# Optimization experiments

Hardware: AMD Instinct MI355X
Metric: run time of the kernel (lower is better)

## Reference

```python
import jax, jax.numpy as jnp
import numpy as np

B, T, DIN, P, HID, L = 256, 512, 25, 128, 256, 5
Q = 0.15
EPS = 1e-5


def setup_inputs() -> dict:
    key = jax.random.key(0)
    ks = jax.random.split(key, 12)
    s = 0.05
    return {
        "x": jax.random.normal(ks[0], (B, T, DIN), jnp.float32),
        "lengths": jax.random.randint(ks[1], (B,), 1, T + 1),
        "ln_g": jnp.ones((DIN,), jnp.float32),
        "ln_b": jnp.zeros((DIN,), jnp.float32),
        "w1": jax.random.normal(ks[2], (DIN, P), jnp.float32) * s,
        "b1": jnp.zeros((P,), jnp.float32),
        "w2": jax.random.normal(ks[3], (P, P), jnp.float32) * s,
        "b2": jnp.zeros((P,), jnp.float32),
        "Wih0": jax.random.normal(ks[4], (2, 3 * HID, P), jnp.float32) * s,
        "Whh0": jax.random.normal(ks[5], (2, 3 * HID, HID), jnp.float32) * s,
        "bih0": jnp.zeros((2, 3 * HID), jnp.float32),
        "bhh0": jnp.zeros((2, 3 * HID), jnp.float32),
        "Wih": jax.random.normal(ks[6], (L - 1, 2, 3 * HID, 2 * HID), jnp.float32) * s,
        "Whh": jax.random.normal(ks[7], (L - 1, 2, 3 * HID, HID), jnp.float32) * s,
        "bih": jnp.zeros((L - 1, 2, 3 * HID), jnp.float32),
        "bhh": jnp.zeros((L - 1, 2, 3 * HID), jnp.float32),
        "Wc": jax.random.normal(ks[8], (2 * HID,), jnp.float32) * s,
        "bc": jnp.zeros((), jnp.float32),
    }


def _gru_dir(xs, mask, Wih, Whh, bih, bhh):
    """Masked unidirectional GRU (PyTorch gate convention). xs:[B,T,Din], mask:[B,T] -> [B,T,HID]."""
    xw = jnp.einsum('btd,gd->btg', xs, Wih) + bih  # [B,T,3H] precomputed input gates

    def step(h, inp):
        xw_t, m_t = inp  # [B,3H], [B]
        gh = h @ Whh.T + bhh
        r = jax.nn.sigmoid(xw_t[:, :HID] + gh[:, :HID])
        z = jax.nn.sigmoid(xw_t[:, HID:2 * HID] + gh[:, HID:2 * HID])
        n = jnp.tanh(xw_t[:, 2 * HID:] + r * gh[:, 2 * HID:])
        h_new = (1.0 - z) * n + z * h
        h = jnp.where(m_t[:, None], h_new, h)        # hold state past sequence end (packing)
        return h, jnp.where(m_t[:, None], h, 0.0)    # padded outputs are zero (pad_packed)

    h0 = jnp.zeros((xs.shape[0], HID), xs.dtype)
    _, ys = jax.lax.scan(step, h0, (xw.transpose(1, 0, 2), mask.T))
    return ys.transpose(1, 0, 2)


def reference(x, lengths, ln_g, ln_b, w1, b1, w2, b2,
              Wih0, Whh0, bih0, bhh0, Wih, Whh, bih, bhh, Wc, bc):
    mask = jnp.arange(T)[None, :] < lengths[:, None]  # [B,T]

    # InputProjection: LayerNorm -> Linear -> GELU(exact) -> Linear
    mu = x.mean(-1, keepdims=True)
    var = ((x - mu) ** 2).mean(-1, keepdims=True)
    xn = (x - mu) / jnp.sqrt(var + EPS) * ln_g + ln_b
    h = jax.nn.gelu(xn @ w1 + b1, approximate=False) @ w2 + b2  # [B,T,P]

    # per-sample time reversal indices (reverse valid prefix only)
    rev = jnp.clip(lengths[:, None] - 1 - jnp.arange(T)[None, :], 0, T - 1)  # [B,T]

    inp = h
    for l in range(L):
        Wi = Wih0 if l == 0 else Wih[l - 1]
        Wh = Whh0 if l == 0 else Whh[l - 1]
        bi = bih0 if l == 0 else bih[l - 1]
        bh = bhh0 if l == 0 else bhh[l - 1]
        yf = _gru_dir(inp, mask, Wi[0], Wh[0], bi[0], bh[0])
        x_rev = jnp.take_along_axis(inp, rev[:, :, None], axis=1) * mask[:, :, None]
        yb_rev = _gru_dir(x_rev, mask, Wi[1], Wh[1], bi[1], bh[1])
        yb = jnp.take_along_axis(yb_rev, rev[:, :, None], axis=1) * mask[:, :, None]
        inp = jnp.concatenate([yf, yb], axis=-1)  # [B,T,2H]
    H = inp

    # TopQPooling: per-sample variable-k top-k by L2-norm score, then mean
    scores = jnp.where(mask, jnp.linalg.norm(H, axis=2), -1e9)
    k_vals = jnp.maximum(jnp.ceil(lengths.astype(jnp.float32) * Q).astype(jnp.int32), 1)  # [B]
    order = jnp.argsort(-scores, axis=1)                      # descending by score
    topmask = jnp.arange(T)[None, :] < k_vals[:, None]        # first k of sorted order
    Hs = jnp.take_along_axis(H, order[:, :, None], axis=1)
    pooled = (Hs * topmask[:, :, None]).sum(axis=1) / k_vals[:, None].astype(H.dtype)

    logits = pooled @ Wc + bc  # [B]
    return logits
```

## Files before the change

kernel.cpp:

```cpp
#include <hip/hip_runtime.h>
#include <math.h>


#define CH 64

__global__ __launch_bounds__(256)
void sort_k(const int* __restrict__ len, int* __restrict__ perm,
            int* __restrict__ nchp, int Bg)
{
    __shared__ int ll[256];
    __shared__ int lp[256];
    const int i = threadIdx.x;
    const int li = len[i];
    ll[i] = li;
    __syncthreads();
    int rk = 0;
    for (int j = 0; j < 256; j++) {
        int lj = ll[j];
        rk += (lj < li || (lj == li && j < i)) ? 1 : 0;
    }
    lp[rk] = i;
    __syncthreads();
    perm[i] = lp[i];
    const int ngrp = 256 / Bg;
    if (i < ngrp) {
        int mx = ll[lp[i * Bg + Bg - 1]];
        int nch = (mx + 63) >> 6;
        nchp[i] = nch < 1 ? 1 : (nch > 8 ? 8 : nch);
    }
}

__global__ __launch_bounds__(256)
void prep_whhT_k(const float* __restrict__ Whh0, const float* __restrict__ Whh,
                 float* __restrict__ out)
{
    int id = blockIdx.x * 256 + threadIdx.x;
    int u = id / 196608, rr = id % 196608;
    int k = rr / 768, c = rr % 768;
    int l = u >> 1, d = u & 1;
    out[id] = (l == 0) ? Whh0[(size_t)(d * 768 + c) * 256 + k]
                       : Whh[(size_t)(((l - 1) * 2 + d) * 768 + c) * 256 + k];
}

__global__ __launch_bounds__(128)
void input_proj_k(const float* __restrict__ x, const int* __restrict__ lengths,
                  const int* __restrict__ perm,
                  const float* __restrict__ lng, const float* __restrict__ lnb,
                  const float* __restrict__ w1, const float* __restrict__ b1v,
                  const float* __restrict__ w2, const float* __restrict__ b2v,
                  float* __restrict__ out, int g0)
{
    const int btl = blockIdx.x;
    const int sl  = btl >> 9;
    const int t   = btl & 511;
    const int b   = perm[g0 + sl];
    if (t >= lengths[b]) return;
    const int tid = threadIdx.x;
    __shared__ float xs[25];
    __shared__ float xn[25];
    __shared__ float hs[128];
    if (tid < 25) xs[tid] = x[((size_t)b * 512 + t) * 25 + tid];
    __syncthreads();
    if (tid < 25) {
        float mu = 0.f;
        #pragma unroll
        for (int k = 0; k < 25; k++) mu += xs[k];
        mu *= (1.f / 25.f);
        float var = 0.f;
        #pragma unroll
        for (int k = 0; k < 25; k++) { float dd = xs[k] - mu; var += dd * dd; }
        var *= (1.f / 25.f);
        float rstd = 1.f / sqrtf(var + 1e-5f);
        xn[tid] = (xs[tid] - mu) * rstd * lng[tid] + lnb[tid];
    }
    __syncthreads();
    float a = b1v[tid];
    #pragma unroll
    for (int k = 0; k < 25; k++) a = fmaf(xn[k], w1[k * 128 + tid], a);
    float ge = 0.5f * a * (1.f + erff(a * 0.70710678118654752440f));
    hs[tid] = ge;
    __syncthreads();
    float o = b2v[tid];
    #pragma unroll 8
    for (int k = 0; k < 128; k++) o = fmaf(hs[k], w2[k * 128 + tid], o);
    out[(size_t)btl * 128 + tid] = o;
}

__global__ __launch_bounds__(256)
void round_k(const float* __restrict__ A, int K,
             const float* __restrict__ W,
             const float* __restrict__ bi,
             const int* __restrict__ lengths, const int* __restrict__ perm,
             const int* __restrict__ nchp, int gidx, int g0, int Bg,
             float* __restrict__ xw_w,
             const float* __restrict__ xw_r,
             const float* __restrict__ whhT,
             const float* __restrict__ bhh,
             float* __restrict__ Y,
             float* __restrict__ hstate,
             int NR, int r)
{
    __shared__ float As[8][68];
    __shared__ float Bs[8][132];
    __shared__ float h_s[260];
    __shared__ float gs[4][776];

    const int tid = threadIdx.x;
    const int nch = nchp[gidx];

    if ((int)blockIdx.x < NR) {
        if (r == 0) return;
        const int d   = ((int)blockIdx.x >= Bg) ? 1 : 0;
        const int s   = (int)blockIdx.x - d * Bg;
        const int lo  = d ? (nch - r) * 64 : (r - 1) * 64;
        if (lo < 0 || lo >= 512) return;
        const int len = lengths[perm[g0 + s]];
        int nst = min(lo + CH, len) - lo;
        if (nst < 0) nst = 0;
        const int first = (r == 1);
        if (!first && nst <= 0) return;

        float* hg = hstate + (size_t)(d * Bg + s) * 256;
        h_s[tid] = first ? 0.f : hg[tid];
        __syncthreads();

        const int kq  = tid >> 6;
        const int q4  = (tid & 63) * 4;
        const float* Wd  = whhT + (size_t)d * 196608;
        const float* xwd = xw_r + (size_t)(d * Bg + s) * 64 * 768;
        const float bh0 = bhh[d * 768 + tid];
        const float bh1 = bhh[d * 768 + 256 + tid];
        const float bh2 = bhh[d * 768 + 512 + tid];

        for (int st = 0; st < nst; st++) {
            const int p = d ? (lo + nst - 1 - st) : (lo + st);
            float a0[4] = {}, a1[4] = {}, a2[4] = {};
            const float* wk = Wd + (size_t)(kq * 64) * 768 + q4;
            #pragma unroll 4
            for (int k4 = 0; k4 < 16; k4++) {
                float4 h4 = *(const float4*)&h_s[kq * 64 + k4 * 4];
                const float* w0 = wk + (size_t)(k4 * 4) * 768;
                float hk[4] = {h4.x, h4.y, h4.z, h4.w};
                #pragma unroll
                for (int kk = 0; kk < 4; kk++) {
                    const float* wr = w0 + (size_t)kk * 768;
                    float4 wv0 = *(const float4*)(wr);
                    float4 wv1 = *(const float4*)(wr + 256);
                    float4 wv2 = *(const float4*)(wr + 512);
                    float h = hk[kk];
                    a0[0] = fmaf(h, wv0.x, a0[0]); a0[1] = fmaf(h, wv0.y, a0[1]);
                    a0[2] = fmaf(h, wv0.z, a0[2]); a0[3] = fmaf(h, wv0.w, a0[3]);
                    a1[0] = fmaf(h, wv1.x, a1[0]); a1[1] = fmaf(h, wv1.y, a1[1]);
                    a1[2] = fmaf(h, wv1.z, a1[2]); a1[3] = fmaf(h, wv1.w, a1[3]);
                    a2[0] = fmaf(h, wv2.x, a2[0]); a2[1] = fmaf(h, wv2.y, a2[1]);
                    a2[2] = fmaf(h, wv2.z, a2[2]); a2[3] = fmaf(h, wv2.w, a2[3]);
                }
            }
            *(float4*)&gs[kq][q4]       = make_float4(a0[0], a0[1], a0[2], a0[3]);
            *(float4*)&gs[kq][256 + q4] = make_float4(a1[0], a1[1], a1[2], a1[3]);
            *(float4*)&gs[kq][512 + q4] = make_float4(a2[0], a2[1], a2[2], a2[3]);
            __syncthreads();
            float gr = bh0 + gs[0][tid] + gs[1][tid] + gs[2][tid] + gs[3][tid];
            float gz = bh1 + gs[0][256 + tid] + gs[1][256 + tid]
                           + gs[2][256 + tid] + gs[3][256 + tid];
            float gn = bh2 + gs[0][512 + tid] + gs[1][512 + tid]
                           + gs[2][512 + tid] + gs[3][512 + tid];
            const float* xr = xwd + (size_t)(p - lo) * 768;
            float rg = 1.f / (1.f + expf(-(xr[tid] + gr)));
            float zg = 1.f / (1.f + expf(-(xr[256 + tid] + gz)));
            float ng = tanhf(xr[512 + tid] + rg * gn);
            float hv = h_s[tid];
            float hn = (1.f - zg) * ng + zg * hv;
            h_s[tid] = hn;
            Y[((size_t)(s * 512 + p)) * 512 + d * 256 + tid] = hn;
            __syncthreads();
        }
        hg[tid] = h_s[tid];
    } else {
        const int gid  = blockIdx.x - NR;
        const int nt   = gid % 6;
        const int rest = gid / 6;
        const int d    = (rest >= Bg) ? 1 : 0;
        const int s    = rest - d * Bg;
        const int lo   = d ? (nch - 1 - r) * 64 : r * 64;
        if (lo < 0 || lo >= 512) return;
        if (lengths[perm[g0 + s]] <= lo) return;

        float acc[4][8] = {};
        const int tm = tid >> 4;
        const int tn = tid & 15;
        const int arr = tid >> 2, ak = (tid & 3) * 2;
        const int bn = tid >> 1, bk = (tid & 1) * 4;

        const float* Ap = A + (size_t)(s * 512 + lo + arr) * K + ak;
        const float* Wp = W + ((size_t)d * 768 + nt * 128 + bn) * K + bk;

        for (int k0 = 0; k0 < K; k0 += 8) {
            float2 av = *(const float2*)(Ap + k0);
            float4 bv = *(const float4*)(Wp + k0);
            __syncthreads();
            As[ak][arr] = av.x; As[ak + 1][arr] = av.y;
            Bs[bk + 0][bn] = bv.x; Bs[bk + 1][bn] = bv.y;
            Bs[bk + 2][bn] = bv.z; Bs[bk + 3][bn] = bv.w;
            __syncthreads();
            #pragma unroll
            for (int kk = 0; kk < 8; kk++) {
                float4 a4 = *(const float4*)&As[kk][tm * 4];
                float4 b0v = *(const float4*)&Bs[kk][tn * 4];
                float4 b1v = *(const float4*)&Bs[kk][64 + tn * 4];
                float ar4[4] = {a4.x, a4.y, a4.z, a4.w};
                float br[8] = {b0v.x, b0v.y, b0v.z, b0v.w,
                               b1v.x, b1v.y, b1v.z, b1v.w};
                #pragma unroll
                for (int i = 0; i < 4; i++)
                    #pragma unroll
                    for (int j = 0; j < 8; j++)
                        acc[i][j] = fmaf(ar4[i], br[j], acc[i][j]);
            }
        }
        const int cb = d * 768 + nt * 128;
        float bv0[4], bv1[4];
        #pragma unroll
        for (int j = 0; j < 4; j++) {
            bv0[j] = bi[cb + tn * 4 + j];
            bv1[j] = bi[cb + 64 + tn * 4 + j];
        }
        #pragma unroll
        for (int i = 0; i < 4; i++) {
            const int row = tm * 4 + i;
            float* o = xw_w + (size_t)((d * Bg + s) * 64 + row) * 768 + nt * 128 + tn * 4;
            float4 c0 = make_float4(acc[i][0] + bv0[0], acc[i][1] + bv0[1],
                                    acc[i][2] + bv0[2], acc[i][3] + bv0[3]);
            float4 c1 = make_float4(acc[i][4] + bv1[0], acc[i][5] + bv1[1],
                                    acc[i][6] + bv1[2], acc[i][7] + bv1[3]);
            *(float4*)(o)      = c0;
            *(float4*)(o + 64) = c1;
        }
    }
}

__global__ __launch_bounds__(256)
void pool_k(const float* __restrict__ H, const int* __restrict__ lengths,
            const int* __restrict__ perm,
            const float* __restrict__ Wc, const float* __restrict__ bcp,
            float* __restrict__ out, int g0)
{
    const int bl = blockIdx.x;
    const int b  = perm[g0 + bl];
    const int tid = threadIdx.x;
    __shared__ float sc[512];
    __shared__ int   sel[128];
    __shared__ int   nsel;
    __shared__ float red[256];
    const int len = lengths[b];
    const int k = max(1, (int)ceilf((float)len * 0.15f));
    if (tid == 0) nsel = 0;
    for (int t = tid; t < 512; t += 256) {
        float s;
        if (t < len) {
            const float* row = H + ((size_t)bl * 512 + t) * 512;
            float acc = 0.f;
            for (int j = 0; j < 512; j++) acc = fmaf(row[j], row[j], acc);
            s = sqrtf(acc);
        } else s = -1e9f;
        sc[t] = s;
    }
    __syncthreads();
    for (int t = tid; t < 512; t += 256) {
        if (t < len) {
            const float s = sc[t];
            int cnt = 0;
            for (int u = 0; u < 512; u++) {
                float su = sc[u];
                cnt += (su > s || (su == s && u < t)) ? 1 : 0;
            }
            if (cnt < k) { int p = atomicAdd(&nsel, 1); sel[p] = t; }
        }
    }
    __syncthreads();
    const int ns = nsel;
    float part = 0.f;
    for (int j = tid; j < 512; j += 256) {
        float acc = 0.f;
        for (int i = 0; i < ns; i++)
            acc += H[((size_t)bl * 512 + sel[i]) * 512 + j];
        part += (acc / (float)k) * Wc[j];
    }
    red[tid] = part;
    __syncthreads();
    for (int s2 = 128; s2 > 0; s2 >>= 1) {
        if (tid < s2) red[tid] += red[tid + s2];
        __syncthreads();
    }
    if (tid == 0) out[b] = red[0] + bcp[0];
}

static inline size_t alup(size_t x) { return (x + 255) & ~255ull; }

static size_t tier_bytes(int Bg)
{
    return 2 * alup((size_t)Bg * 512 * 512 * 4)
         + 2 * alup((size_t)Bg * 2 * 64 * 768 * 4)
         + alup(1966080ull * 4)
         + alup((size_t)Bg * 2 * 256 * 4)
         + alup(2048);
}

extern "C" void kernel_launch(void* const* d_in, const int* in_sizes, int n_in,
                              void* d_out, int out_size, void* d_ws, size_t ws_size,
                              hipStream_t stream)
{
    const float* x    = (const float*)d_in[0];
    const int*   len  = (const int*)  d_in[1];
    const float* ln_g = (const float*)d_in[2];
    const float* ln_b = (const float*)d_in[3];
    const float* w1   = (const float*)d_in[4];
    const float* b1   = (const float*)d_in[5];
    const float* w2   = (const float*)d_in[6];
    const float* b2   = (const float*)d_in[7];
    const float* Wih0 = (const float*)d_in[8];
    const float* Whh0 = (const float*)d_in[9];
    const float* bih0 = (const float*)d_in[10];
    const float* bhh0 = (const float*)d_in[11];
    const float* Wih  = (const float*)d_in[12];
    const float* Whh  = (const float*)d_in[13];
    const float* bih  = (const float*)d_in[14];
    const float* bhh  = (const float*)d_in[15];
    const float* Wc   = (const float*)d_in[16];
    const float* bc   = (const float*)d_in[17];
    float* out = (float*)d_out;

    int Bg = 0;
    const int tiers[5] = {128, 64, 32, 16, 8};
    for (int i = 0; i < 5; i++)
        if (ws_size >= tier_bytes(tiers[i])) { Bg = tiers[i]; break; }
    if (Bg == 0) return;

    char* ws = (char*)d_ws;
    size_t off = 0;
    auto alloc = [&](size_t bytes) { size_t o = off; off += alup(bytes); return o; };
    float* h0    = (float*)(ws + alloc((size_t)Bg * 512 * 512 * 4));
    float* h1    = (float*)(ws + alloc((size_t)Bg * 512 * 512 * 4));
    float* xwA   = (float*)(ws + alloc((size_t)Bg * 2 * 64 * 768 * 4));
    float* xwB   = (float*)(ws + alloc((size_t)Bg * 2 * 64 * 768 * 4));
    float* whhT  = (float*)(ws + alloc(1966080ull * 4));
    float* hst   = (float*)(ws + alloc((size_t)Bg * 2 * 256 * 4));
    int*   perm  = (int*)  (ws + alloc(2048));
    int*   nchp  = perm + 256;
    float* xwbuf[2] = {xwA, xwB};

    sort_k<<<1, 256, 0, stream>>>(len, perm, nchp, Bg);
    prep_whhT_k<<<7680, 256, 0, stream>>>(Whh0, Whh, whhT);

    const int NR = 2 * Bg;
    const int NG = 12 * Bg;

    for (int g0 = 0; g0 < 256; g0 += Bg) {
        const int gidx = g0 / Bg;
        input_proj_k<<<Bg * 512, 128, 0, stream>>>(x, len, perm, ln_g, ln_b,
                                                   w1, b1, w2, b2, h0, g0);
        float* bin = h0;
        float* bout = h1;
        for (int l = 0; l < 5; l++) {
            const int K = (l == 0) ? 128 : 512;
            const float* Wl  = (l == 0) ? Wih0 : (Wih + (size_t)(l - 1) * 2 * 768 * 512);
            const float* bil = (l == 0) ? bih0 : (bih + (size_t)(l - 1) * 1536);
            const float* whl = whhT + (size_t)l * 393216;
            const float* bhl = (l == 0) ? bhh0 : (bhh + (size_t)(l - 1) * 1536);
            for (int r = 0; r <= 8; r++) {
                round_k<<<NR + NG, 256, 0, stream>>>(
                    bin, K, Wl, bil, len, perm, nchp, gidx, g0, Bg,
                    xwbuf[r & 1], xwbuf[(r & 1) ^ 1],
                    whl, bhl, bout, hst, NR, r);
            }
            float* tmp = bin; bin = bout; bout = tmp;
        }
        pool_k<<<Bg, 256, 0, stream>>>(bin, len, perm, Wc, bc, out, g0);
    }
}
```

Measured before the change: 49.20 ms.

## Batch four sequences per recurrent block and widen input-projection GEMM tiles

The recurrent blocks now process four sequences at once, with one thread per hidden unit doing the full K=256 dot product. Each Whh weight load is reused across four hidden states, and the cross-warp gate reduction in shared memory is removed. The input-projection GEMM moves to 128x128 tiles with 8x8 register blocking across several sequences. Workspace tiers now allow a group of all 256 sequences with configurable chunk length, and empty phases launch fewer blocks. This trades more registers per thread and fewer recurrent blocks for less weight bandwidth per step, and it assumes sorted lengths so that sequences in a tile are similar.

```diff
diff --git a/kernel.cpp b/kernel.cpp
--- a/kernel.cpp
+++ b/kernel.cpp
@@ -2,11 +2,9 @@
 #include <math.h>
 
 
-#define CH 64
-
 __global__ __launch_bounds__(256)
 void sort_k(const int* __restrict__ len, int* __restrict__ perm,
-            int* __restrict__ nchp, int Bg)
+            int* __restrict__ nchp, int Bg, int CHv)
 {
     __shared__ int ll[256];
     __shared__ int lp[256];
@@ -23,10 +21,11 @@
     __syncthreads();
     perm[i] = lp[i];
     const int ngrp = 256 / Bg;
+    const int rmax = 512 / CHv;
     if (i < ngrp) {
         int mx = ll[lp[i * Bg + Bg - 1]];
-        int nch = (mx + 63) >> 6;
-        nchp[i] = nch < 1 ? 1 : (nch > 8 ? 8 : nch);
+        int nch = (mx + CHv - 1) / CHv;
+        nchp[i] = nch < 1 ? 1 : (nch > rmax ? rmax : nch);
     }
 }
 
@@ -92,6 +91,7 @@
              const float* __restrict__ bi,
              const int* __restrict__ lengths, const int* __restrict__ perm,
              const int* __restrict__ nchp, int gidx, int g0, int Bg,
+             int CHv, int chsh,
              float* __restrict__ xw_w,
              const float* __restrict__ xw_r,
              const float* __restrict__ whhT,
@@ -100,141 +100,154 @@
              float* __restrict__ hstate,
              int NR, int r)
 {
-    __shared__ float As[8][68];
+    __shared__ float As[8][132];
     __shared__ float Bs[8][132];
-    __shared__ float h_s[260];
-    __shared__ float gs[4][776];
+    __shared__ float h_s[2][256][4];
 
     const int tid = threadIdx.x;
     const int nch = nchp[gidx];
 
     if ((int)blockIdx.x < NR) {
-        if (r == 0) return;
-        const int d   = ((int)blockIdx.x >= Bg) ? 1 : 0;
-        const int s   = (int)blockIdx.x - d * Bg;
-        const int lo  = d ? (nch - r) * 64 : (r - 1) * 64;
+        const int half = NR >> 1;
+        const int d    = ((int)blockIdx.x >= half) ? 1 : 0;
+        const int tile = (int)blockIdx.x - d * half;
+        const int b0   = tile * 4;
+        const int lo   = d ? (nch - r) * CHv : (r - 1) * CHv;
         if (lo < 0 || lo >= 512) return;
-        const int len = lengths[perm[g0 + s]];
-        int nst = min(lo + CH, len) - lo;
-        if (nst < 0) nst = 0;
         const int first = (r == 1);
-        if (!first && nst <= 0) return;
-
-        float* hg = hstate + (size_t)(d * Bg + s) * 256;
-        h_s[tid] = first ? 0.f : hg[tid];
+
+        int nst[4];
+        int nmax = 0;
+        #pragma unroll
+        for (int s = 0; s < 4; s++) {
+            int L = lengths[perm[g0 + b0 + s]];
+            int n = min(lo + CHv, L) - lo;
+            nst[s] = (n < 0) ? 0 : n;
+            nmax = max(nmax, nst[s]);
+        }
+        if (!first && nmax <= 0) return;
+
+        const int j = tid;
+        float* hg = hstate + (size_t)(d * Bg + b0) * 256;
+        #pragma unroll
+        for (int s = 0; s < 4; s++)
+            h_s[0][j][s] = first ? 0.f : hg[s * 256 + j];
         __syncthreads();
 
-        const int kq  = tid >> 6;
-        const int q4  = (tid & 63) * 4;
         const float* Wd  = whhT + (size_t)d * 196608;
-        const float* xwd = xw_r + (size_t)(d * Bg + s) * 64 * 768;
-        const float bh0 = bhh[d * 768 + tid];
-        const float bh1 = bhh[d * 768 + 256 + tid];
-        const float bh2 = bhh[d * 768 + 512 + tid];
-
-        for (int st = 0; st < nst; st++) {
-            const int p = d ? (lo + nst - 1 - st) : (lo + st);
-            float a0[4] = {}, a1[4] = {}, a2[4] = {};
-            const float* wk = Wd + (size_t)(kq * 64) * 768 + q4;
+        const float* xwd = xw_r + (size_t)(d * Bg + b0) * ((size_t)CHv * 768);
+        const float bh0 = bhh[d * 768 + j];
+        const float bh1 = bhh[d * 768 + 256 + j];
+        const float bh2 = bhh[d * 768 + 512 + j];
+
+        int par = 0;
+        for (int st = 0; st < nmax; st++) {
+            float ar[4] = {}, az[4] = {}, an[4] = {};
+            const float* wp = Wd + j;
             #pragma unroll 4
-            for (int k4 = 0; k4 < 16; k4++) {
-                float4 h4 = *(const float4*)&h_s[kq * 64 + k4 * 4];
-                const float* w0 = wk + (size_t)(k4 * 4) * 768;
-                float hk[4] = {h4.x, h4.y, h4.z, h4.w};
-                #pragma unroll
-                for (int kk = 0; kk < 4; kk++) {
-                    const float* wr = w0 + (size_t)kk * 768;
-                    float4 wv0 = *(const float4*)(wr);
-                    float4 wv1 = *(const float4*)(wr + 256);
-                    float4 wv2 = *(const float4*)(wr + 512);
-                    float h = hk[kk];
-                    a0[0] = fmaf(h, wv0.x, a0[0]); a0[1] = fmaf(h, wv0.y, a0[1]);
-                    a0[2] = fmaf(h, wv0.z, a0[2]); a0[3] = fmaf(h, wv0.w, a0[3]);
-                    a1[0] = fmaf(h, wv1.x, a1[0]); a1[1] = fmaf(h, wv1.y, a1[1]);
-                    a1[2] = fmaf(h, wv1.z, a1[2]); a1[3] = fmaf(h, wv1.w, a1[3]);
-                    a2[0] = fmaf(h, wv2.x, a2[0]); a2[1] = fmaf(h, wv2.y, a2[1]);
-                    a2[2] = fmaf(h, wv2.z, a2[2]); a2[3] = fmaf(h, wv2.w, a2[3]);
+            for (int k = 0; k < 256; k++) {
+                float wr = wp[0];
+                float wz = wp[256];
+                float wn = wp[512];
+                wp += 768;
+                float4 h4 = *(const float4*)&h_s[par][k][0];
+                ar[0] = fmaf(h4.x, wr, ar[0]); ar[1] = fmaf(h4.y, wr, ar[1]);
+                ar[2] = fmaf(h4.z, wr, ar[2]); ar[3] = fmaf(h4.w, wr, ar[3]);
+                az[0] = fmaf(h4.x, wz, az[0]); az[1] = fmaf(h4.y, wz, az[1]);
+                az[2] = fmaf(h4.z, wz, az[2]); az[3] = fmaf(h4.w, wz, az[3]);
+                an[0] = fmaf(h4.x, wn, an[0]); an[1] = fmaf(h4.y, wn, an[1]);
+                an[2] = fmaf(h4.z, wn, an[2]); an[3] = fmaf(h4.w, wn, an[3]);
+            }
+            float4 hv4 = *(const float4*)&h_s[par][j][0];
+            float hold[4] = {hv4.x, hv4.y, hv4.z, hv4.w};
+            float hnew[4];
+            #pragma unroll
+            for (int s = 0; s < 4; s++) {
+                float hn = hold[s];
+                if (st < nst[s]) {
+                    int p = d ? (lo + nst[s] - 1 - st) : (lo + st);
+                    const float* xr = xwd + ((size_t)s * CHv + (p - lo)) * 768;
+                    float rg = 1.f / (1.f + expf(-(xr[j] + ar[s] + bh0)));
+                    float zg = 1.f / (1.f + expf(-(xr[256 + j] + az[s] + bh1)));
+                    float ng = tanhf(xr[512 + j] + rg * (an[s] + bh2));
+                    hn = (1.f - zg) * ng + zg * hold[s];
+                    Y[((size_t)((b0 + s) * 512 + p)) * 512 + d * 256 + j] = hn;
                 }
-            }
-            *(float4*)&gs[kq][q4]       = make_float4(a0[0], a0[1], a0[2], a0[3]);
-            *(float4*)&gs[kq][256 + q4] = make_float4(a1[0], a1[1], a1[2], a1[3]);
-            *(float4*)&gs[kq][512 + q4] = make_float4(a2[0], a2[1], a2[2], a2[3]);
+                hnew[s] = hn;
+            }
+            *(float4*)&h_s[par ^ 1][j][0] =
+                make_float4(hnew[0], hnew[1], hnew[2], hnew[3]);
+            par ^= 1;
             __syncthreads();
-            float gr = bh0 + gs[0][tid] + gs[1][tid] + gs[2][tid] + gs[3][tid];
-            float gz = bh1 + gs[0][256 + tid] + gs[1][256 + tid]
-                           + gs[2][256 + tid] + gs[3][256 + tid];
-            float gn = bh2 + gs[0][512 + tid] + gs[1][512 + tid]
-                           + gs[2][512 + tid] + gs[3][512 + tid];
-            const float* xr = xwd + (size_t)(p - lo) * 768;
-            float rg = 1.f / (1.f + expf(-(xr[tid] + gr)));
-            float zg = 1.f / (1.f + expf(-(xr[256 + tid] + gz)));
-            float ng = tanhf(xr[512 + tid] + rg * gn);
-            float hv = h_s[tid];
-            float hn = (1.f - zg) * ng + zg * hv;
-            h_s[tid] = hn;
-            Y[((size_t)(s * 512 + p)) * 512 + d * 256 + tid] = hn;
-            __syncthreads();
-        }
-        hg[tid] = h_s[tid];
+        }
+        #pragma unroll
+        for (int s = 0; s < 4; s++) hg[s * 256 + j] = h_s[par][j][s];
     } else {
         const int gid  = blockIdx.x - NR;
         const int nt   = gid % 6;
         const int rest = gid / 6;
-        const int d    = (rest >= Bg) ? 1 : 0;
-        const int s    = rest - d * Bg;
-        const int lo   = d ? (nch - 1 - r) * 64 : r * 64;
+        const int nRT  = (Bg << 1) * CHv >> 7;
+        const int hRT  = nRT >> 1;
+        const int dirg = (rest >= hRT) ? 1 : 0;
+        const int rt   = rest - dirg * hRT;
+        const int spt  = 128 >> chsh;
+        const int s0   = rt * spt;
+        const int lo   = dirg ? (nch - 1 - r) * CHv : r * CHv;
         if (lo < 0 || lo >= 512) return;
-        if (lengths[perm[g0 + s]] <= lo) return;
-
-        float acc[4][8] = {};
-        const int tm = tid >> 4;
-        const int tn = tid & 15;
-        const int arr = tid >> 2, ak = (tid & 3) * 2;
-        const int bn = tid >> 1, bk = (tid & 1) * 4;
-
-        const float* Ap = A + (size_t)(s * 512 + lo + arr) * K + ak;
-        const float* Wp = W + ((size_t)d * 768 + nt * 128 + bn) * K + bk;
+        if (lengths[perm[g0 + s0 + spt - 1]] <= lo) return;
+
+        float acc[8][8] = {};
+        const int tx8 = (tid & 15) << 3;
+        const int ty8 = (tid >> 4) << 3;
+        const int am  = tid >> 1;
+        const int ah  = (tid & 1) << 2;
+        const int cb  = dirg * 768 + nt * 128;
+
+        const int sA = s0 + (am >> chsh);
+        const int pA = lo + (am & (CHv - 1));
+        const float* Ap = A + ((size_t)sA * 512 + pA) * K + ah;
+        const float* Wp = W + ((size_t)cb + am) * K + ah;
 
         for (int k0 = 0; k0 < K; k0 += 8) {
-            float2 av = *(const float2*)(Ap + k0);
+            float4 av = *(const float4*)(Ap + k0);
             float4 bv = *(const float4*)(Wp + k0);
             __syncthreads();
-            As[ak][arr] = av.x; As[ak + 1][arr] = av.y;
-            Bs[bk + 0][bn] = bv.x; Bs[bk + 1][bn] = bv.y;
-            Bs[bk + 2][bn] = bv.z; Bs[bk + 3][bn] = bv.w;
+            As[ah + 0][am] = av.x; As[ah + 1][am] = av.y;
+            As[ah + 2][am] = av.z; As[ah + 3][am] = av.w;
+            Bs[ah + 0][am] = bv.x; Bs[ah + 1][am] = bv.y;
+            Bs[ah + 2][am] = bv.z; Bs[ah + 3][am] = bv.w;
             __syncthreads();
             #pragma unroll
             for (int kk = 0; kk < 8; kk++) {
-                float4 a4 = *(const float4*)&As[kk][tm * 4];
-                float4 b0v = *(const float4*)&Bs[kk][tn * 4];
-                float4 b1v = *(const float4*)&Bs[kk][64 + tn * 4];
-                float ar4[4] = {a4.x, a4.y, a4.z, a4.w};
-                float br[8] = {b0v.x, b0v.y, b0v.z, b0v.w,
-                               b1v.x, b1v.y, b1v.z, b1v.w};
+                float4 a0 = *(const float4*)&As[kk][ty8];
+                float4 a1 = *(const float4*)&As[kk][ty8 + 4];
+                float4 b0 = *(const float4*)&Bs[kk][tx8];
+                float4 b1 = *(const float4*)&Bs[kk][tx8 + 4];
+                float ax[8] = {a0.x, a0.y, a0.z, a0.w, a1.x, a1.y, a1.z, a1.w};
+                float bx[8] = {b0.x, b0.y, b0.z, b0.w, b1.x, b1.y, b1.z, b1.w};
                 #pragma unroll
-                for (int i = 0; i < 4; i++)
+                for (int i = 0; i < 8; i++)
                     #pragma unroll
-                    for (int j = 0; j < 8; j++)
-                        acc[i][j] = fmaf(ar4[i], br[j], acc[i][j]);
-            }
-        }
-        const int cb = d * 768 + nt * 128;
-        float bv0[4], bv1[4];
-        #pragma unroll
-        for (int j = 0; j < 4; j++) {
-            bv0[j] = bi[cb + tn * 4 + j];
-            bv1[j] = bi[cb + 64 + tn * 4 + j];
-        }
-        #pragma unroll
-        for (int i = 0; i < 4; i++) {
-            const int row = tm * 4 + i;
-            float* o = xw_w + (size_t)((d * Bg + s) * 64 + row) * 768 + nt * 128 + tn * 4;
-            float4 c0 = make_float4(acc[i][0] + bv0[0], acc[i][1] + bv0[1],
-                                    acc[i][2] + bv0[2], acc[i][3] + bv0[3]);
-            float4 c1 = make_float4(acc[i][4] + bv1[0], acc[i][5] + bv1[1],
-                                    acc[i][6] + bv1[2], acc[i][7] + bv1[3]);
-            *(float4*)(o)      = c0;
-            *(float4*)(o + 64) = c1;
+                    for (int jj = 0; jj < 8; jj++)
+                        acc[i][jj] = fmaf(ax[i], bx[jj], acc[i][jj]);
+            }
+        }
+        float bsv[8];
+        #pragma unroll
+        for (int jj = 0; jj < 8; jj++) bsv[jj] = bi[cb + tx8 + jj];
+        #pragma unroll
+        for (int i = 0; i < 8; i++) {
+            const int row = ty8 + i;
+            const int sl  = s0 + (row >> chsh);
+            const int po  = row & (CHv - 1);
+            float* o = xw_w + (size_t)((dirg * Bg + sl) * CHv + po) * 768
+                     + nt * 128 + tx8;
+            float4 c0 = make_float4(acc[i][0] + bsv[0], acc[i][1] + bsv[1],
+                                    acc[i][2] + bsv[2], acc[i][3] + bsv[3]);
+            float4 c1 = make_float4(acc[i][4] + bsv[4], acc[i][5] + bsv[5],
+                                    acc[i][6] + bsv[6], acc[i][7] + bsv[7]);
+            *(float4*)(o)     = c0;
+            *(float4*)(o + 4) = c1;
         }
     }
 }
@@ -297,10 +310,10 @@
 
 static inline size_t alup(size_t x) { return (x + 255) & ~255ull; }
 
-static size_t tier_bytes(int Bg)
+static size_t tier_bytes(int Bg, int CHv)
 {
     return 2 * alup((size_t)Bg * 512 * 512 * 4)
-         + 2 * alup((size_t)Bg * 2 * 64 * 768 * 4)
+         + 2 * alup((size_t)Bg * 2 * CHv * 768 * 4)
          + alup(1966080ull * 4)
          + alup((size_t)Bg * 2 * 256 * 4)
          + alup(2048);
@@ -330,30 +343,33 @@
     const float* bc   = (const float*)d_in[17];
     float* out = (float*)d_out;
 
-    int Bg = 0;
-    const int tiers[5] = {128, 64, 32, 16, 8};
-    for (int i = 0; i < 5; i++)
-        if (ws_size >= tier_bytes(tiers[i])) { Bg = tiers[i]; break; }
+    const int tBg[7] = {256, 256, 128, 128, 64, 32, 16};
+    const int tCH[7] = { 64,  32,  64,  32, 64, 64, 64};
+    int Bg = 0, CHv = 64;
+    for (int i = 0; i < 7; i++)
+        if (ws_size >= tier_bytes(tBg[i], tCH[i])) { Bg = tBg[i]; CHv = tCH[i]; break; }
     if (Bg == 0) return;
+    const int chsh = (CHv == 64) ? 6 : 5;
+    const int RMAX = 512 / CHv;
 
     char* ws = (char*)d_ws;
     size_t off = 0;
     auto alloc = [&](size_t bytes) { size_t o = off; off += alup(bytes); return o; };
-    float* h0    = (float*)(ws + alloc((size_t)Bg * 512 * 512 * 4));
-    float* h1    = (float*)(ws + alloc((size_t)Bg * 512 * 512 * 4));
-    float* xwA   = (float*)(ws + alloc((size_t)Bg * 2 * 64 * 768 * 4));
-    float* xwB   = (float*)(ws + alloc((size_t)Bg * 2 * 64 * 768 * 4));
-    float* whhT  = (float*)(ws + alloc(1966080ull * 4));
-    float* hst   = (float*)(ws + alloc((size_t)Bg * 2 * 256 * 4));
-    int*   perm  = (int*)  (ws + alloc(2048));
-    int*   nchp  = perm + 256;
+    float* h0   = (float*)(ws + alloc((size_t)Bg * 512 * 512 * 4));
+    float* h1   = (float*)(ws + alloc((size_t)Bg * 512 * 512 * 4));
+    float* xwA  = (float*)(ws + alloc((size_t)Bg * 2 * CHv * 768 * 4));
+    float* xwB  = (float*)(ws + alloc((size_t)Bg * 2 * CHv * 768 * 4));
+    float* whhT = (float*)(ws + alloc(1966080ull * 4));
+    float* hst  = (float*)(ws + alloc((size_t)Bg * 2 * 256 * 4));
+    int*   perm = (int*)  (ws + alloc(2048));
+    int*   nchp = perm + 256;
     float* xwbuf[2] = {xwA, xwB};
 
-    sort_k<<<1, 256, 0, stream>>>(len, perm, nchp, Bg);
+    sort_k<<<1, 256, 0, stream>>>(len, perm, nchp, Bg, CHv);
     prep_whhT_k<<<7680, 256, 0, stream>>>(Whh0, Whh, whhT);
 
-    const int NR = 2 * Bg;
-    const int NG = 12 * Bg;
+    const int NRfull = Bg / 2;
+    const int NGfull = 6 * ((Bg * 2 * CHv) >> 7);
 
     for (int g0 = 0; g0 < 256; g0 += Bg) {
         const int gidx = g0 / Bg;
@@ -367,9 +383,11 @@
             const float* bil = (l == 0) ? bih0 : (bih + (size_t)(l - 1) * 1536);
             const float* whl = whhT + (size_t)l * 393216;
             const float* bhl = (l == 0) ? bhh0 : (bhh + (size_t)(l - 1) * 1536);
-            for (int r = 0; r <= 8; r++) {
+            for (int r = 0; r <= RMAX; r++) {
+                const int NR = (r > 0) ? NRfull : 0;
+                const int NG = (r < RMAX) ? NGfull : 0;
                 round_k<<<NR + NG, 256, 0, stream>>>(
-                    bin, K, Wl, bil, len, perm, nchp, gidx, g0, Bg,
+                    bin, K, Wl, bil, len, perm, nchp, gidx, g0, Bg, CHv, chsh,
                     xwbuf[r & 1], xwbuf[(r & 1) ^ 1],
                     whl, bhl, bout, hst, NR, r);
             }
```

Result: slower. 99.31 ms (+101.8%).

## Process two sequences per recurrent block and allow configurable chunk length

Applied to the files above, without the earlier changes.

Each recurrent block now advances two sorted sequences at once, so every Whh weight load from memory feeds two hidden-state matvecs, halving weight traffic per step. The chunk length becomes a runtime parameter (64 or 32), and the tier table now allows the whole batch of 256 in one group when workspace permits. The GEMM tiles are remapped so a 64-row tile can span several sequences when chunks are 32. Launches also drop the empty recurrent or GEMM half in the first and last rounds. The costs are padding steps when the two paired lengths differ, twice the register accumulators, and more rounds when chunks are shorter.

```diff
diff --git a/kernel.cpp b/kernel.cpp
--- a/kernel.cpp
+++ b/kernel.cpp
@@ -2,11 +2,9 @@
 #include <math.h>
 
 
-#define CH 64
-
 __global__ __launch_bounds__(256)
 void sort_k(const int* __restrict__ len, int* __restrict__ perm,
-            int* __restrict__ nchp, int Bg)
+            int* __restrict__ nchp, int Bg, int CHv)
 {
     __shared__ int ll[256];
     __shared__ int lp[256];
@@ -23,10 +21,11 @@
     __syncthreads();
     perm[i] = lp[i];
     const int ngrp = 256 / Bg;
+    const int rmax = 512 / CHv;
     if (i < ngrp) {
         int mx = ll[lp[i * Bg + Bg - 1]];
-        int nch = (mx + 63) >> 6;
-        nchp[i] = nch < 1 ? 1 : (nch > 8 ? 8 : nch);
+        int nch = (mx + CHv - 1) / CHv;
+        nchp[i] = nch < 1 ? 1 : (nch > rmax ? rmax : nch);
     }
 }
 
@@ -92,6 +91,7 @@
              const float* __restrict__ bi,
              const int* __restrict__ lengths, const int* __restrict__ perm,
              const int* __restrict__ nchp, int gidx, int g0, int Bg,
+             int CHv, int chsh,
              float* __restrict__ xw_w,
              const float* __restrict__ xw_r,
              const float* __restrict__ whhT,
@@ -102,89 +102,121 @@
 {
     __shared__ float As[8][68];
     __shared__ float Bs[8][132];
-    __shared__ float h_s[260];
-    __shared__ float gs[4][776];
+    __shared__ float h_s[2][260];
+    __shared__ float gs[2][4][776];
 
     const int tid = threadIdx.x;
     const int nch = nchp[gidx];
 
     if ((int)blockIdx.x < NR) {
-        if (r == 0) return;
-        const int d   = ((int)blockIdx.x >= Bg) ? 1 : 0;
-        const int s   = (int)blockIdx.x - d * Bg;
-        const int lo  = d ? (nch - r) * 64 : (r - 1) * 64;
+        const int half = NR >> 1;
+        const int d    = ((int)blockIdx.x >= half) ? 1 : 0;
+        const int pr   = (int)blockIdx.x - d * half;
+        const int b0   = pr * 2;
+        const int lo   = d ? (nch - r) * CHv : (r - 1) * CHv;
         if (lo < 0 || lo >= 512) return;
-        const int len = lengths[perm[g0 + s]];
-        int nst = min(lo + CH, len) - lo;
-        if (nst < 0) nst = 0;
         const int first = (r == 1);
-        if (!first && nst <= 0) return;
-
-        float* hg = hstate + (size_t)(d * Bg + s) * 256;
-        h_s[tid] = first ? 0.f : hg[tid];
+
+        int nst[2];
+        #pragma unroll
+        for (int s = 0; s < 2; s++) {
+            int L = lengths[perm[g0 + b0 + s]];
+            int n = min(lo + CHv, L) - lo;
+            nst[s] = (n < 0) ? 0 : n;
+        }
+        const int nmax = max(nst[0], nst[1]);
+        if (!first && nmax <= 0) return;
+
+        float* hg = hstate + (size_t)(d * Bg + b0) * 256;
+        h_s[0][tid] = first ? 0.f : hg[tid];
+        h_s[1][tid] = first ? 0.f : hg[256 + tid];
         __syncthreads();
 
         const int kq  = tid >> 6;
         const int q4  = (tid & 63) * 4;
         const float* Wd  = whhT + (size_t)d * 196608;
-        const float* xwd = xw_r + (size_t)(d * Bg + s) * 64 * 768;
+        const float* xwd = xw_r + (size_t)(d * Bg + b0) * ((size_t)CHv * 768);
         const float bh0 = bhh[d * 768 + tid];
         const float bh1 = bhh[d * 768 + 256 + tid];
         const float bh2 = bhh[d * 768 + 512 + tid];
 
-        for (int st = 0; st < nst; st++) {
-            const int p = d ? (lo + nst - 1 - st) : (lo + st);
-            float a0[4] = {}, a1[4] = {}, a2[4] = {};
+        for (int st = 0; st < nmax; st++) {
+            float a0[2][4] = {}, a1[2][4] = {}, a2[2][4] = {};
             const float* wk = Wd + (size_t)(kq * 64) * 768 + q4;
             #pragma unroll 4
             for (int k4 = 0; k4 < 16; k4++) {
-                float4 h4 = *(const float4*)&h_s[kq * 64 + k4 * 4];
+                const int kb = kq * 64 + k4 * 4;
+                float ha[4], hb[4];
+                #pragma unroll
+                for (int kk = 0; kk < 4; kk++) {
+                    ha[kk] = h_s[0][kb + kk];
+                    hb[kk] = h_s[1][kb + kk];
+                }
                 const float* w0 = wk + (size_t)(k4 * 4) * 768;
-                float hk[4] = {h4.x, h4.y, h4.z, h4.w};
                 #pragma unroll
                 for (int kk = 0; kk < 4; kk++) {
                     const float* wr = w0 + (size_t)kk * 768;
                     float4 wv0 = *(const float4*)(wr);
                     float4 wv1 = *(const float4*)(wr + 256);
                     float4 wv2 = *(const float4*)(wr + 512);
-                    float h = hk[kk];
-                    a0[0] = fmaf(h, wv0.x, a0[0]); a0[1] = fmaf(h, wv0.y, a0[1]);
-                    a0[2] = fmaf(h, wv0.z, a0[2]); a0[3] = fmaf(h, wv0.w, a0[3]);
-                    a1[0] = fmaf(h, wv1.x, a1[0]); a1[1] = fmaf(h, wv1.y, a1[1]);
-                    a1[2] = fmaf(h, wv1.z, a1[2]); a1[3] = fmaf(h, wv1.w, a1[3]);
-                    a2[0] = fmaf(h, wv2.x, a2[0]); a2[1] = fmaf(h, wv2.y, a2[1]);
-                    a2[2] = fmaf(h, wv2.z, a2[2]); a2[3] = fmaf(h, wv2.w, a2[3]);
+                    float u = ha[kk], v = hb[kk];
+                    a0[0][0] = fmaf(u, wv0.x, a0[0][0]); a0[0][1] = fmaf(u, wv0.y, a0[0][1]);
+                    a0[0][2] = fmaf(u, wv0.z, a0[0][2]); a0[0][3] = fmaf(u, wv0.w, a0[0][3]);
+                    a1[0][0] = fmaf(u, wv1.x, a1[0][0]); a1[0][1] = fmaf(u, wv1.y, a1[0][1]);
+                    a1[0][2] = fmaf(u, wv1.z, a1[0][2]); a1[0][3] = fmaf(u, wv1.w, a1[0][3]);
+                    a2[0][0] = fmaf(u, wv2.x, a2[0][0]); a2[0][1] = fmaf(u, wv2.y, a2[0][1]);
+                    a2[0][2] = fmaf(u, wv2.z, a2[0][2]); a2[0][3] = fmaf(u, wv2.w, a2[0][3]);
+                    a0[1][0] = fmaf(v, wv0.x, a0[1][0]); a0[1][1] = fmaf(v, wv0.y, a0[1][1]);
+                    a0[1][2] = fmaf(v, wv0.z, a0[1][2]); a0[1][3] = fmaf(v, wv0.w, a0[1][3]);
+                    a1[1][0] = fmaf(v, wv1.x, a1[1][0]); a1[1][1] = fmaf(v, wv1.y, a1[1][1]);
+                    a1[1][2] = fmaf(v, wv1.z, a1[1][2]); a1[1][3] = fmaf(v, wv1.w, a1[1][3]);
+                    a2[1][0] = fmaf(v, wv2.x, a2[1][0]); a2[1][1] = fmaf(v, wv2.y, a2[1][1]);
+                    a2[1][2] = fmaf(v, wv2.z, a2[1][2]); a2[1][3] = fmaf(v, wv2.w, a2[1][3]);
                 }
             }
-            *(float4*)&gs[kq][q4]       = make_float4(a0[0], a0[1], a0[2], a0[3]);
-            *(float4*)&gs[kq][256 + q4] = make_float4(a1[0], a1[1], a1[2], a1[3]);
-            *(float4*)&gs[kq][512 + q4] = make_float4(a2[0], a2[1], a2[2], a2[3]);
+            #pragma unroll
+            for (int s = 0; s < 2; s++) {
+                *(float4*)&gs[s][kq][q4]       = make_float4(a0[s][0], a0[s][1], a0[s][2], a0[s][3]);
+                *(float4*)&gs[s][kq][256 + q4] = make_float4(a1[s][0], a1[s][1], a1[s][2], a1[s][3]);
+                *(float4*)&gs[s][kq][512 + q4] = make_float4(a2[s][0], a2[s][1], a2[s][2], a2[s][3]);
+            }
             __syncthreads();
-            float gr = bh0 + gs[0][tid] + gs[1][tid] + gs[2][tid] + gs[3][tid];
-            float gz = bh1 + gs[0][256 + tid] + gs[1][256 + tid]
-                           + gs[2][256 + tid] + gs[3][256 + tid];
-            float gn = bh2 + gs[0][512 + tid] + gs[1][512 + tid]
-                           + gs[2][512 + tid] + gs[3][512 + tid];
-            const float* xr = xwd + (size_t)(p - lo) * 768;
-            float rg = 1.f / (1.f + expf(-(xr[tid] + gr)));
-            float zg = 1.f / (1.f + expf(-(xr[256 + tid] + gz)));
-            float ng = tanhf(xr[512 + tid] + rg * gn);
-            float hv = h_s[tid];
-            float hn = (1.f - zg) * ng + zg * hv;
-            h_s[tid] = hn;
-            Y[((size_t)(s * 512 + p)) * 512 + d * 256 + tid] = hn;
+            #pragma unroll
+            for (int s = 0; s < 2; s++) {
+                if (st < nst[s]) {
+                    const int p = d ? (lo + nst[s] - 1 - st) : (lo + st);
+                    float gr = bh0 + gs[s][0][tid] + gs[s][1][tid]
+                                   + gs[s][2][tid] + gs[s][3][tid];
+                    float gz = bh1 + gs[s][0][256 + tid] + gs[s][1][256 + tid]
+                                   + gs[s][2][256 + tid] + gs[s][3][256 + tid];
+                    float gn = bh2 + gs[s][0][512 + tid] + gs[s][1][512 + tid]
+                                   + gs[s][2][512 + tid] + gs[s][3][512 + tid];
+                    const float* xr = xwd + ((size_t)s * CHv + (p - lo)) * 768;
+                    float rg = 1.f / (1.f + expf(-(xr[tid] + gr)));
+                    float zg = 1.f / (1.f + expf(-(xr[256 + tid] + gz)));
+                    float ng = tanhf(xr[512 + tid] + rg * gn);
+                    float hv = h_s[s][tid];
+                    float hn = (1.f - zg) * ng + zg * hv;
+                    h_s[s][tid] = hn;
+                    Y[((size_t)((b0 + s) * 512 + p)) * 512 + d * 256 + tid] = hn;
+                }
+            }
             __syncthreads();
         }
-        hg[tid] = h_s[tid];
+        hg[tid]       = h_s[0][tid];
+        hg[256 + tid] = h_s[1][tid];
     } else {
         const int gid  = blockIdx.x - NR;
         const int nt   = gid % 6;
         const int rest = gid / 6;
-        const int d    = (rest >= Bg) ? 1 : 0;
-        const int s    = rest - d * Bg;
-        const int lo   = d ? (nch - 1 - r) * 64 : r * 64;
+        const int spt  = 64 >> chsh;
+        const int tpd  = Bg / spt;
+        const int dd   = (rest >= tpd) ? 1 : 0;
+        const int rt   = rest - dd * tpd;
+        const int s0   = rt * spt;
+        const int lo   = dd ? (nch - 1 - r) * CHv : r * CHv;
         if (lo < 0 || lo >= 512) return;
-        if (lengths[perm[g0 + s]] <= lo) return;
+        if (lengths[perm[g0 + s0 + spt - 1]] <= lo) return;
 
         float acc[4][8] = {};
         const int tm = tid >> 4;
@@ -192,8 +224,10 @@
         const int arr = tid >> 2, ak = (tid & 3) * 2;
         const int bn = tid >> 1, bk = (tid & 1) * 4;
 
-        const float* Ap = A + (size_t)(s * 512 + lo + arr) * K + ak;
-        const float* Wp = W + ((size_t)d * 768 + nt * 128 + bn) * K + bk;
+        const int sA = s0 + (arr >> chsh);
+        const int pA = lo + (arr & (CHv - 1));
+        const float* Ap = A + ((size_t)sA * 512 + pA) * K + ak;
+        const float* Wp = W + ((size_t)dd * 768 + nt * 128 + bn) * K + bk;
 
         for (int k0 = 0; k0 < K; k0 += 8) {
             float2 av = *(const float2*)(Ap + k0);
@@ -218,7 +252,7 @@
                         acc[i][j] = fmaf(ar4[i], br[j], acc[i][j]);
             }
         }
-        const int cb = d * 768 + nt * 128;
+        const int cb = dd * 768 + nt * 128;
         float bv0[4], bv1[4];
         #pragma unroll
         for (int j = 0; j < 4; j++) {
@@ -228,7 +262,10 @@
         #pragma unroll
         for (int i = 0; i < 4; i++) {
             const int row = tm * 4 + i;
-            float* o = xw_w + (size_t)((d * Bg + s) * 64 + row) * 768 + nt * 128 + tn * 4;
+            const int sl  = s0 + (row >> chsh);
+            const int po  = row & (CHv - 1);
+            float* o = xw_w + (size_t)((dd * Bg + sl) * CHv + po) * 768
+                     + nt * 128 + tn * 4;
             float4 c0 = make_float4(acc[i][0] + bv0[0], acc[i][1] + bv0[1],
                                     acc[i][2] + bv0[2], acc[i][3] + bv0[3]);
             float4 c1 = make_float4(acc[i][4] + bv1[0], acc[i][5] + bv1[1],
@@ -297,10 +334,10 @@
 
 static inline size_t alup(size_t x) { return (x + 255) & ~255ull; }
 
-static size_t tier_bytes(int Bg)
+static size_t tier_bytes(int Bg, int CHv)
 {
     return 2 * alup((size_t)Bg * 512 * 512 * 4)
-         + 2 * alup((size_t)Bg * 2 * 64 * 768 * 4)
+         + 2 * alup((size_t)Bg * 2 * CHv * 768 * 4)
          + alup(1966080ull * 4)
          + alup((size_t)Bg * 2 * 256 * 4)
          + alup(2048);
@@ -330,30 +367,33 @@
     const float* bc   = (const float*)d_in[17];
     float* out = (float*)d_out;
 
-    int Bg = 0;
-    const int tiers[5] = {128, 64, 32, 16, 8};
-    for (int i = 0; i < 5; i++)
-        if (ws_size >= tier_bytes(tiers[i])) { Bg = tiers[i]; break; }
+    const int tBg[7] = {256, 256, 128, 128, 64, 32, 16};
+    const int tCH[7] = { 64,  32,  64,  32, 64, 64, 64};
+    int Bg = 0, CHv = 64;
+    for (int i = 0; i < 7; i++)
+        if (ws_size >= tier_bytes(tBg[i], tCH[i])) { Bg = tBg[i]; CHv = tCH[i]; break; }
     if (Bg == 0) return;
+    const int chsh = (CHv == 64) ? 6 : 5;
+    const int RMAX = 512 / CHv;
 
     char* ws = (char*)d_ws;
     size_t off = 0;
     auto alloc = [&](size_t bytes) { size_t o = off; off += alup(bytes); return o; };
-    float* h0    = (float*)(ws + alloc((size_t)Bg * 512 * 512 * 4));
-    float* h1    = (float*)(ws + alloc((size_t)Bg * 512 * 512 * 4));
-    float* xwA   = (float*)(ws + alloc((size_t)Bg * 2 * 64 * 768 * 4));
-    float* xwB   = (float*)(ws + alloc((size_t)Bg * 2 * 64 * 768 * 4));
-    float* whhT  = (float*)(ws + alloc(1966080ull * 4));
-    float* hst   = (float*)(ws + alloc((size_t)Bg * 2 * 256 * 4));
-    int*   perm  = (int*)  (ws + alloc(2048));
-    int*   nchp  = perm + 256;
+    float* h0   = (float*)(ws + alloc((size_t)Bg * 512 * 512 * 4));
+    float* h1   = (float*)(ws + alloc((size_t)Bg * 512 * 512 * 4));
+    float* xwA  = (float*)(ws + alloc((size_t)Bg * 2 * CHv * 768 * 4));
+    float* xwB  = (float*)(ws + alloc((size_t)Bg * 2 * CHv * 768 * 4));
+    float* whhT = (float*)(ws + alloc(1966080ull * 4));
+    float* hst  = (float*)(ws + alloc((size_t)Bg * 2 * 256 * 4));
+    int*   perm = (int*)  (ws + alloc(2048));
+    int*   nchp = perm + 256;
     float* xwbuf[2] = {xwA, xwB};
 
-    sort_k<<<1, 256, 0, stream>>>(len, perm, nchp, Bg);
+    sort_k<<<1, 256, 0, stream>>>(len, perm, nchp, Bg, CHv);
     prep_whhT_k<<<7680, 256, 0, stream>>>(Whh0, Whh, whhT);
 
-    const int NR = 2 * Bg;
-    const int NG = 12 * Bg;
+    const int NRfull = Bg;
+    const int NGfull = 6 * 2 * Bg * CHv / 64;
 
     for (int g0 = 0; g0 < 256; g0 += Bg) {
         const int gidx = g0 / Bg;
@@ -367,9 +407,11 @@
             const float* bil = (l == 0) ? bih0 : (bih + (size_t)(l - 1) * 1536);
             const float* whl = whhT + (size_t)l * 393216;
             const float* bhl = (l == 0) ? bhh0 : (bhh + (size_t)(l - 1) * 1536);
-            for (int r = 0; r <= 8; r++) {
+            for (int r = 0; r <= RMAX; r++) {
+                const int NR = (r > 0) ? NRfull : 0;
+                const int NG = (r < RMAX) ? NGfull : 0;
                 round_k<<<NR + NG, 256, 0, stream>>>(
-                    bin, K, Wl, bil, len, perm, nchp, gidx, g0, Bg,
+                    bin, K, Wl, bil, len, perm, nchp, gidx, g0, Bg, CHv, chsh,
                     xwbuf[r & 1], xwbuf[(r & 1) ^ 1],
                     whl, bhl, bout, hst, NR, r);
             }
```

New measurement: 95.22 ms. 1.94x slower.
